# Kernel optimization log

Hardware: AMD Instinct MI355X
Metric: run time of the kernel (lower is better)

## Reference

```python
import jax, jax.numpy as jnp
import numpy as np

EPS = 1e-6

def setup_inputs() -> dict:
    key = jax.random.key(0)
    S, U, D = 512, 32, 512
    dvecs = jax.random.normal(key, (S, U, D), dtype=jnp.float32)
    w = jnp.array([10.0], dtype=jnp.float32)
    b = jnp.array([-5.0], dtype=jnp.float32)
    return {"dvecs": dvecs, "w": w, "b": b}


def _ge2e_loss(dvecs, w, b):
    S, U, D = dvecs.shape
    # Full centroids [S, D]
    centroids = dvecs.mean(axis=1)
    # Leave-one-out centroids [S, U, D] (equivalent to the roll/unfold/mean trick)
    loo = (dvecs.sum(axis=1, keepdims=True) - dvecs) / (U - 1)
    # Norms, clamped like F.cosine_similarity eps
    dn = jnp.linalg.norm(dvecs, axis=-1)        # [S, U]
    cn = jnp.linalg.norm(centroids, axis=-1)    # [S]
    ln = jnp.linalg.norm(loo, axis=-1)          # [S, U]
    # Cosine sim of every utterance vs every speaker centroid: [S, U, S]
    sim_all = jnp.einsum('sud,jd->suj', dvecs, centroids) / jnp.maximum(dn[..., None] * cn[None, None, :], EPS)
    # Self-speaker column uses the leave-one-out centroid (index_copy in torch code)
    sim_self = jnp.einsum('sud,sud->su', dvecs, loo) / jnp.maximum(dn * ln, EPS)
    spk = jnp.arange(S)
    self_mask = spk[:, None, None] == spk[None, None, :]          # [S, 1, S] -> broadcasts to [S, U, S]
    sim = jnp.where(self_mask, sim_self[..., None], sim_all)
    logits = sim * w[0] + b[0]
    losses = -jax.nn.log_softmax(logits, axis=2)                  # [S, U, S]
    # Select losses[s, u, s] and sum (index_select of diagonal entries)
    return jnp.sum(jnp.where(self_mask, losses, 0.0))


def reference(dvecs, w, b):
    return _ge2e_loss(dvecs, w, b)
```

## Files before the change

kernel.cpp:

```cpp
#include <hip/hip_runtime.h>
#include <math.h>

#define NS 512
#define NU 32
#define ND 512
#define GEPS 1e-6f

typedef float f4 __attribute__((ext_vector_type(4)));
typedef _Float16 half8 __attribute__((ext_vector_type(8)));


__global__ __launch_bounds__(256) void prep_full(const float* __restrict__ dvecs,
                                                 _Float16* __restrict__ bpk,
                                                 float* __restrict__ cn2,
                                                 float* __restrict__ dn2,
                                                 _Float16* __restrict__ apk) {
    const int s = blockIdx.x, t = threadIdx.x;
    const int l = t & 63, w = t >> 6, l15 = l & 15, lg = l >> 4;
    const int rt = w >> 1, tkh = (w & 1) * 8;
    const float* base = dvecs + (size_t)s * NU * ND;
    __shared__ float dn2p[4][16];
    __shared__ float red[4];

    const int u = rt * 16 + l15;
    const float* rowp = base + (size_t)u * ND;
    float q = 0.f;
    #pragma unroll
    for (int i = 0; i < 8; ++i) {
        const int tk = tkh + i;
        const int k0 = tk * 32 + lg * 8;
        f4 a0 = *(const f4*)(rowp + k0);
        f4 a1 = *(const f4*)(rowp + k0 + 4);
        q += a0[0]*a0[0] + a0[1]*a0[1] + a0[2]*a0[2] + a0[3]*a0[3]
           + a1[0]*a1[0] + a1[1]*a1[1] + a1[2]*a1[2] + a1[3]*a1[3];
        half8 h, lo;
        #pragma unroll
        for (int c = 0; c < 4; ++c) {
            _Float16 h0 = (_Float16)a0[c];
            h[c]     = h0; lo[c]     = (_Float16)(a0[c] - (float)h0);
            _Float16 h1 = (_Float16)a1[c];
            h[4 + c] = h1; lo[4 + c] = (_Float16)(a1[c] - (float)h1);
        }
        _Float16* cb = apk + ((size_t)(s * 2 + rt) * 16 + tk) * 1024 + l * 8;
        *(half8*)cb         = h;
        *(half8*)(cb + 512) = lo;
    }
    q += __shfl_xor(q, 16);
    q += __shfl_xor(q, 32);
    if (lg == 0) dn2p[w][l15] = q;

    const int d0 = t * 2;
    float sx = 0.f, sy = 0.f;
    #pragma unroll 4
    for (int u2 = 0; u2 < NU; ++u2) {
        float2 v = *(const float2*)(base + u2 * ND + d0);
        sx += v.x; sy += v.y;
    }
    sx *= (1.0f / NU); sy *= (1.0f / NU);
    float c2 = sx * sx + sy * sy;
    #pragma unroll
    for (int m = 1; m < 64; m <<= 1) c2 += __shfl_xor(c2, m);
    if ((t & 63) == 0) red[t >> 6] = c2;
    __syncthreads();
    if (t < 32)
        dn2[s * NU + t] = dn2p[(t >> 4) * 2][t & 15] + dn2p[(t >> 4) * 2 + 1][t & 15];
    if (t == 0) cn2[s] = red[0] + red[1] + red[2] + red[3];

    _Float16 hx = (_Float16)sx, hy = (_Float16)sy;
    _Float16 lx = (_Float16)(sx - (float)hx), ly = (_Float16)(sy - (float)hy);
    const int ct_g = s >> 4, cl15 = s & 15;
    const int tt = d0 >> 5, blg = (d0 >> 3) & 3, j = d0 & 7;
    size_t hbase = ((size_t)(ct_g * 16 + tt)) * 1024 + (blg * 16 + cl15) * 8 + j;
    unsigned hi2 = (unsigned)__builtin_bit_cast(unsigned short, hx)
                 | ((unsigned)__builtin_bit_cast(unsigned short, hy) << 16);
    unsigned lo2 = (unsigned)__builtin_bit_cast(unsigned short, lx)
                 | ((unsigned)__builtin_bit_cast(unsigned short, ly) << 16);
    *(unsigned*)(bpk + hbase)       = hi2;
    *(unsigned*)(bpk + hbase + 512) = lo2;
}

__global__ __launch_bounds__(512, 3) void ge2e_full(const _Float16* __restrict__ apk,
                                                    const _Float16* __restrict__ bpk,
                                                    const float* __restrict__ cn2,
                                                    const float* __restrict__ dn2,
                                                    const float* __restrict__ wp,
                                                    const float* __restrict__ bp,
                                                    float* __restrict__ out) {
    const int s0 = blockIdx.x * 2, tid = threadIdx.x;
    const int l = tid & 63;
    const int wv = __builtin_amdgcn_readfirstlane(tid >> 6);
    const int l15 = l & 15, lg = l >> 4;

    f4 acc[2][2][4];
    #pragma unroll
    for (int sp = 0; sp < 2; ++sp)
        #pragma unroll
        for (int rt = 0; rt < 2; ++rt)
            #pragma unroll
            for (int ct = 0; ct < 4; ++ct) acc[sp][rt][ct] = (f4){0.f, 0.f, 0.f, 0.f};

    const _Float16* Au = apk + (size_t)s0 * 32 * 1024;
    const _Float16* Bu = bpk + (size_t)(wv * 4) * 16 * 1024;
    const int voff = l * 8;

    #pragma unroll 2
    for (int t = 0; t < 16; ++t) {
        half8 bh[4], bl[4];
        #pragma unroll
        for (int ct = 0; ct < 4; ++ct) {
            const _Float16* p = Bu + (ct * 16 + t) * 1024 + voff;
            bh[ct] = *(const half8*)p;
            bl[ct] = *(const half8*)(p + 512);
        }
        #pragma unroll
        for (int sp = 0; sp < 2; ++sp) {
            half8 ah[2], al[2];
            #pragma unroll
            for (int rt = 0; rt < 2; ++rt) {
                const _Float16* p = Au + sp * 32 * 1024 + (rt * 16 + t) * 1024 + voff;
                ah[rt] = *(const half8*)p;
                al[rt] = *(const half8*)(p + 512);
            }
            __builtin_amdgcn_s_setprio(1);
            #pragma unroll
            for (int ct = 0; ct < 4; ++ct)
                #pragma unroll
                for (int rt = 0; rt < 2; ++rt) {
                    acc[sp][rt][ct] = __builtin_amdgcn_mfma_f32_16x16x32_f16(ah[rt], bh[ct], acc[sp][rt][ct], 0, 0, 0);
                    acc[sp][rt][ct] = __builtin_amdgcn_mfma_f32_16x16x32_f16(ah[rt], bl[ct], acc[sp][rt][ct], 0, 0, 0);
                    acc[sp][rt][ct] = __builtin_amdgcn_mfma_f32_16x16x32_f16(al[rt], bh[ct], acc[sp][rt][ct], 0, 0, 0);
                    acc[sp][rt][ct] = __builtin_amdgcn_mfma_f32_16x16x32_f16(al[rt], bl[ct], acc[sp][rt][ct], 0, 0, 0);
                }
            __builtin_amdgcn_s_setprio(0);
        }
    }

    __shared__ float sDn2[2][32], sSelf[2][32], sMax[2][8][32], sSum[2][8][32], sRow[2][32];
    if (tid < 64) sDn2[tid >> 5][tid & 31] = dn2[(s0 + (tid >> 5)) * NU + (tid & 31)];
    __syncthreads();

    const float w = wp[0], bb = bp[0];

    #pragma unroll
    for (int sp = 0; sp < 2; ++sp) {
        const int s = s0 + sp;
        const float cn2s = cn2[s];
        float dv[2][4];
        #pragma unroll
        for (int rt = 0; rt < 2; ++rt)
            #pragma unroll
            for (int r = 0; r < 4; ++r) dv[rt][r] = sDn2[sp][rt * 16 + lg * 4 + r];

        const bool owner = (wv == (s >> 6)) && (l15 == (s & 15));
        const int  ctd   = (s >> 4) & 3;

        float dotc[2][4];
        #pragma unroll
        for (int ct = 0; ct < 4; ++ct)
            if (ct == ctd)
                #pragma unroll
                for (int rt = 0; rt < 2; ++rt)
                    #pragma unroll
                    for (int r = 0; r < 4; ++r) dotc[rt][r] = acc[sp][rt][ct][r];

        #pragma unroll
        for (int ct = 0; ct < 4; ++ct) {
            const float cv = cn2[wv * 64 + ct * 16 + l15];
            #pragma unroll
            for (int rt = 0; rt < 2; ++rt)
                #pragma unroll
                for (int r = 0; r < 4; ++r)
                    acc[sp][rt][ct][r] = w * (acc[sp][rt][ct][r] / fmaxf(sqrtf(dv[rt][r] * cv), GEPS)) + bb;
        }
        if (owner) {
            #pragma unroll
            for (int rt = 0; rt < 2; ++rt)
                #pragma unroll
                for (int r = 0; r < 4; ++r) {
                    const float d2  = dv[rt][r];
                    const float num = (float)NU * dotc[rt][r] - d2;
                    const float X   = (float)(NU * NU) * cn2s - 2.0f * NU * dotc[rt][r] + d2;
                    const float den = fmaxf(sqrtf(d2) * sqrtf(X), GEPS * (NU - 1));
                    const float ls  = w * (num / den) + bb;
                    #pragma unroll
                    for (int ct = 0; ct < 4; ++ct)
                        if (ct == ctd) acc[sp][rt][ct][r] = ls;
                    sSelf[sp][rt * 16 + lg * 4 + r] = ls;
                }
        }

        #pragma unroll
        for (int rt = 0; rt < 2; ++rt)
            #pragma unroll
            for (int r = 0; r < 4; ++r) {
                float mx = -INFINITY;
                #pragma unroll
                for (int ct = 0; ct < 4; ++ct) mx = fmaxf(mx, acc[sp][rt][ct][r]);
                mx = fmaxf(mx, __shfl_xor(mx, 1)); mx = fmaxf(mx, __shfl_xor(mx, 2));
                mx = fmaxf(mx, __shfl_xor(mx, 4)); mx = fmaxf(mx, __shfl_xor(mx, 8));
                float se = 0.f;
                #pragma unroll
                for (int ct = 0; ct < 4; ++ct) se += expf(acc[sp][rt][ct][r] - mx);
                se += __shfl_xor(se, 1); se += __shfl_xor(se, 2);
                se += __shfl_xor(se, 4); se += __shfl_xor(se, 8);
                if (l15 == 0) {
                    sMax[sp][wv][rt * 16 + lg * 4 + r] = mx;
                    sSum[sp][wv][rt * 16 + lg * 4 + r] = se;
                }
            }
    }
    __syncthreads();

    if (tid < 64) {
        const int sp = tid >> 5, u2 = tid & 31;
        float M = -INFINITY;
        #pragma unroll
        for (int v = 0; v < 8; ++v) M = fmaxf(M, sMax[sp][v][u2]);
        float S = 0.f;
        #pragma unroll
        for (int v = 0; v < 8; ++v) S += sSum[sp][v][u2] * expf(sMax[sp][v][u2] - M);
        sRow[sp][u2] = logf(S) + M - sSelf[sp][u2];
    }
    __syncthreads();
    if (tid == 0) {
        float tot = 0.f;
        #pragma unroll
        for (int sp = 0; sp < 2; ++sp)
            #pragma unroll
            for (int u2 = 0; u2 < 32; ++u2) tot += sRow[sp][u2];
        atomicAdd(out, tot);
    }
}

extern "C" void kernel_launch(void* const* d_in, const int* in_sizes, int n_in,
                              void* d_out, int out_size, void* d_ws, size_t ws_size,
                              hipStream_t stream) {
    const float* dvecs = (const float*)d_in[0];
    const float* w     = (const float*)d_in[1];
    const float* b     = (const float*)d_in[2];
    float* out = (float*)d_out;

    const size_t bpk_b = (size_t)32 * 16 * 1024 * sizeof(_Float16);
    const size_t cn2_b = (size_t)NS * sizeof(float);
    const size_t dn2_b = (size_t)NS * NU * sizeof(float);

    char* p = (char*)d_ws;
    _Float16* bpk = (_Float16*)p;                 p += bpk_b;
    float*    cn2 = (float*)p;                    p += cn2_b;
    float*    dn2 = (float*)p;                    p += dn2_b;
    _Float16* apk = (_Float16*)p;

    hipMemsetAsync(d_out, 0, sizeof(float), stream);
    prep_full<<<NS, 256, 0, stream>>>(dvecs, bpk, cn2, dn2, apk);
    ge2e_full<<<NS / 2, 512, 0, stream>>>(apk, bpk, cn2, dn2, w, b, out);
}
```

Measured before the change: 130.6 us.

## Split prep kernel, one speaker per GEMM block, double-buffer B fragments

The fused prep kernel is split in two. One kernel packs the fp16 hi/lo A tiles and row norms over 2x more blocks, and a separate kernel computes centroids and their packed form. The main kernel now handles one speaker per block instead of two, doubling the grid to 512 blocks, and the occupancy hint rises to 4. The K loop is fully unrolled with B fragments prefetched one step ahead. This adds parallelism and latency hiding, at the cost of an extra launch, a second read of dvecs, and each block re-reading the B data for only one speaker.

```diff
diff --git a/kernel.cpp b/kernel.cpp
--- a/kernel.cpp
+++ b/kernel.cpp
@@ -10,24 +10,19 @@
 typedef _Float16 half8 __attribute__((ext_vector_type(8)));
 
 
-__global__ __launch_bounds__(256) void prep_full(const float* __restrict__ dvecs,
-                                                 _Float16* __restrict__ bpk,
-                                                 float* __restrict__ cn2,
-                                                 float* __restrict__ dn2,
-                                                 _Float16* __restrict__ apk) {
-    const int s = blockIdx.x, t = threadIdx.x;
-    const int l = t & 63, w = t >> 6, l15 = l & 15, lg = l >> 4;
-    const int rt = w >> 1, tkh = (w & 1) * 8;
-    const float* base = dvecs + (size_t)s * NU * ND;
+__global__ __launch_bounds__(256) void prep_apk(const float* __restrict__ dvecs,
+                                                float* __restrict__ dn2,
+                                                _Float16* __restrict__ apk) {
+    const int b = blockIdx.x, s = b >> 1, rt = b & 1;
+    const int t = threadIdx.x, l = t & 63, w = t >> 6, l15 = l & 15, lg = l >> 4;
+    const int u = rt * 16 + l15;
+    const float* rowp = dvecs + ((size_t)s * NU + u) * ND;
     __shared__ float dn2p[4][16];
-    __shared__ float red[4];
-
-    const int u = rt * 16 + l15;
-    const float* rowp = base + (size_t)u * ND;
+
     float q = 0.f;
     #pragma unroll
-    for (int i = 0; i < 8; ++i) {
-        const int tk = tkh + i;
+    for (int i = 0; i < 4; ++i) {
+        const int tk = w * 4 + i;
         const int k0 = tk * 32 + lg * 8;
         f4 a0 = *(const f4*)(rowp + k0);
         f4 a1 = *(const f4*)(rowp + k0 + 4);
@@ -48,22 +43,30 @@
     q += __shfl_xor(q, 16);
     q += __shfl_xor(q, 32);
     if (lg == 0) dn2p[w][l15] = q;
-
+    __syncthreads();
+    if (t < 16)
+        dn2[s * NU + rt * 16 + t] = dn2p[0][t] + dn2p[1][t] + dn2p[2][t] + dn2p[3][t];
+}
+
+__global__ __launch_bounds__(256) void prep_cent(const float* __restrict__ dvecs,
+                                                 _Float16* __restrict__ bpk,
+                                                 float* __restrict__ cn2) {
+    const int s = blockIdx.x, t = threadIdx.x;
+    const float* base = dvecs + (size_t)s * NU * ND;
     const int d0 = t * 2;
     float sx = 0.f, sy = 0.f;
     #pragma unroll 4
-    for (int u2 = 0; u2 < NU; ++u2) {
-        float2 v = *(const float2*)(base + u2 * ND + d0);
+    for (int u = 0; u < NU; ++u) {
+        float2 v = *(const float2*)(base + u * ND + d0);
         sx += v.x; sy += v.y;
     }
     sx *= (1.0f / NU); sy *= (1.0f / NU);
     float c2 = sx * sx + sy * sy;
     #pragma unroll
     for (int m = 1; m < 64; m <<= 1) c2 += __shfl_xor(c2, m);
+    __shared__ float red[4];
     if ((t & 63) == 0) red[t >> 6] = c2;
     __syncthreads();
-    if (t < 32)
-        dn2[s * NU + t] = dn2p[(t >> 4) * 2][t & 15] + dn2p[(t >> 4) * 2 + 1][t & 15];
     if (t == 0) cn2[s] = red[0] + red[1] + red[2] + red[3];
 
     _Float16 hx = (_Float16)sx, hy = (_Float16)sy;
@@ -79,45 +82,50 @@
     *(unsigned*)(bpk + hbase + 512) = lo2;
 }
 
-__global__ __launch_bounds__(512, 3) void ge2e_full(const _Float16* __restrict__ apk,
+__global__ __launch_bounds__(512, 4) void ge2e_full(const _Float16* __restrict__ apk,
                                                     const _Float16* __restrict__ bpk,
                                                     const float* __restrict__ cn2,
                                                     const float* __restrict__ dn2,
                                                     const float* __restrict__ wp,
                                                     const float* __restrict__ bp,
                                                     float* __restrict__ out) {
-    const int s0 = blockIdx.x * 2, tid = threadIdx.x;
+    const int s = blockIdx.x, tid = threadIdx.x;
     const int l = tid & 63;
     const int wv = __builtin_amdgcn_readfirstlane(tid >> 6);
     const int l15 = l & 15, lg = l >> 4;
 
-    f4 acc[2][2][4];
-    #pragma unroll
-    for (int sp = 0; sp < 2; ++sp)
-        #pragma unroll
-        for (int rt = 0; rt < 2; ++rt)
-            #pragma unroll
-            for (int ct = 0; ct < 4; ++ct) acc[sp][rt][ct] = (f4){0.f, 0.f, 0.f, 0.f};
-
-    const _Float16* Au = apk + (size_t)s0 * 32 * 1024;
+    f4 acc[2][4];
+    #pragma unroll
+    for (int rt = 0; rt < 2; ++rt)
+        #pragma unroll
+        for (int ct = 0; ct < 4; ++ct) acc[rt][ct] = (f4){0.f, 0.f, 0.f, 0.f};
+
+    const _Float16* Au = apk + (size_t)s * 32 * 1024;
     const _Float16* Bu = bpk + (size_t)(wv * 4) * 16 * 1024;
     const int voff = l * 8;
 
-    #pragma unroll 2
-    for (int t = 0; t < 16; ++t) {
-        half8 bh[4], bl[4];
+    half8 bh0[4], bl0[4], bh1[4], bl1[4];
+    #pragma unroll
+    for (int ct = 0; ct < 4; ++ct) {
+        const _Float16* p = Bu + (ct * 16 + 0) * 1024 + voff;
+        bh0[ct] = *(const half8*)p;
+        bl0[ct] = *(const half8*)(p + 512);
+    }
+
+    #pragma unroll
+    for (int tt = 0; tt < 8; ++tt) {
+        const int t0 = tt * 2, t1 = t0 + 1;
         #pragma unroll
         for (int ct = 0; ct < 4; ++ct) {
-            const _Float16* p = Bu + (ct * 16 + t) * 1024 + voff;
-            bh[ct] = *(const half8*)p;
-            bl[ct] = *(const half8*)(p + 512);
-        }
-        #pragma unroll
-        for (int sp = 0; sp < 2; ++sp) {
+            const _Float16* p = Bu + (ct * 16 + t1) * 1024 + voff;
+            bh1[ct] = *(const half8*)p;
+            bl1[ct] = *(const half8*)(p + 512);
+        }
+        {
             half8 ah[2], al[2];
             #pragma unroll
             for (int rt = 0; rt < 2; ++rt) {
-                const _Float16* p = Au + sp * 32 * 1024 + (rt * 16 + t) * 1024 + voff;
+                const _Float16* p = Au + (rt * 16 + t0) * 1024 + voff;
                 ah[rt] = *(const half8*)p;
                 al[rt] = *(const half8*)(p + 512);
             }
@@ -126,108 +134,128 @@
             for (int ct = 0; ct < 4; ++ct)
                 #pragma unroll
                 for (int rt = 0; rt < 2; ++rt) {
-                    acc[sp][rt][ct] = __builtin_amdgcn_mfma_f32_16x16x32_f16(ah[rt], bh[ct], acc[sp][rt][ct], 0, 0, 0);
-                    acc[sp][rt][ct] = __builtin_amdgcn_mfma_f32_16x16x32_f16(ah[rt], bl[ct], acc[sp][rt][ct], 0, 0, 0);
-                    acc[sp][rt][ct] = __builtin_amdgcn_mfma_f32_16x16x32_f16(al[rt], bh[ct], acc[sp][rt][ct], 0, 0, 0);
-                    acc[sp][rt][ct] = __builtin_amdgcn_mfma_f32_16x16x32_f16(al[rt], bl[ct], acc[sp][rt][ct], 0, 0, 0);
+                    acc[rt][ct] = __builtin_amdgcn_mfma_f32_16x16x32_f16(ah[rt], bh0[ct], acc[rt][ct], 0, 0, 0);
+                    acc[rt][ct] = __builtin_amdgcn_mfma_f32_16x16x32_f16(ah[rt], bl0[ct], acc[rt][ct], 0, 0, 0);
+                    acc[rt][ct] = __builtin_amdgcn_mfma_f32_16x16x32_f16(al[rt], bh0[ct], acc[rt][ct], 0, 0, 0);
+                    acc[rt][ct] = __builtin_amdgcn_mfma_f32_16x16x32_f16(al[rt], bl0[ct], acc[rt][ct], 0, 0, 0);
                 }
             __builtin_amdgcn_s_setprio(0);
         }
-    }
-
-    __shared__ float sDn2[2][32], sSelf[2][32], sMax[2][8][32], sSum[2][8][32], sRow[2][32];
-    if (tid < 64) sDn2[tid >> 5][tid & 31] = dn2[(s0 + (tid >> 5)) * NU + (tid & 31)];
+        if (tt < 7) {
+            #pragma unroll
+            for (int ct = 0; ct < 4; ++ct) {
+                const _Float16* p = Bu + (ct * 16 + t0 + 2) * 1024 + voff;
+                bh0[ct] = *(const half8*)p;
+                bl0[ct] = *(const half8*)(p + 512);
+            }
+        }
+        {
+            half8 ah[2], al[2];
+            #pragma unroll
+            for (int rt = 0; rt < 2; ++rt) {
+                const _Float16* p = Au + (rt * 16 + t1) * 1024 + voff;
+                ah[rt] = *(const half8*)p;
+                al[rt] = *(const half8*)(p + 512);
+            }
+            __builtin_amdgcn_s_setprio(1);
+            #pragma unroll
+            for (int ct = 0; ct < 4; ++ct)
+                #pragma unroll
+                for (int rt = 0; rt < 2; ++rt) {
+                    acc[rt][ct] = __builtin_amdgcn_mfma_f32_16x16x32_f16(ah[rt], bh1[ct], acc[rt][ct], 0, 0, 0);
+                    acc[rt][ct] = __builtin_amdgcn_mfma_f32_16x16x32_f16(ah[rt], bl1[ct], acc[rt][ct], 0, 0, 0);
+                    acc[rt][ct] = __builtin_amdgcn_mfma_f32_16x16x32_f16(al[rt], bh1[ct], acc[rt][ct], 0, 0, 0);
+                    acc[rt][ct] = __builtin_amdgcn_mfma_f32_16x16x32_f16(al[rt], bl1[ct], acc[rt][ct], 0, 0, 0);
+                }
+            __builtin_amdgcn_s_setprio(0);
+        }
+    }
+
+    __shared__ float sDn2[32], sSelf[32], sMax[8][32], sSum[8][32], sRow[32];
+    if (tid < 32) sDn2[tid] = dn2[s * NU + tid];
     __syncthreads();
 
     const float w = wp[0], bb = bp[0];
-
-    #pragma unroll
-    for (int sp = 0; sp < 2; ++sp) {
-        const int s = s0 + sp;
-        const float cn2s = cn2[s];
-        float dv[2][4];
+    const float cn2s = cn2[s];
+    float dv[2][4];
+    #pragma unroll
+    for (int rt = 0; rt < 2; ++rt)
+        #pragma unroll
+        for (int r = 0; r < 4; ++r) dv[rt][r] = sDn2[rt * 16 + lg * 4 + r];
+
+    const bool owner = (wv == (s >> 6)) && (l15 == (s & 15));
+    const int  ctd   = (s >> 4) & 3;
+
+    float dotc[2][4];
+    #pragma unroll
+    for (int ct = 0; ct < 4; ++ct)
+        if (ct == ctd)
+            #pragma unroll
+            for (int rt = 0; rt < 2; ++rt)
+                #pragma unroll
+                for (int r = 0; r < 4; ++r) dotc[rt][r] = acc[rt][ct][r];
+
+    #pragma unroll
+    for (int ct = 0; ct < 4; ++ct) {
+        const float cv = cn2[wv * 64 + ct * 16 + l15];
         #pragma unroll
         for (int rt = 0; rt < 2; ++rt)
             #pragma unroll
-            for (int r = 0; r < 4; ++r) dv[rt][r] = sDn2[sp][rt * 16 + lg * 4 + r];
-
-        const bool owner = (wv == (s >> 6)) && (l15 == (s & 15));
-        const int  ctd   = (s >> 4) & 3;
-
-        float dotc[2][4];
-        #pragma unroll
-        for (int ct = 0; ct < 4; ++ct)
-            if (ct == ctd)
-                #pragma unroll
-                for (int rt = 0; rt < 2; ++rt)
-                    #pragma unroll
-                    for (int r = 0; r < 4; ++r) dotc[rt][r] = acc[sp][rt][ct][r];
-
-        #pragma unroll
-        for (int ct = 0; ct < 4; ++ct) {
-            const float cv = cn2[wv * 64 + ct * 16 + l15];
-            #pragma unroll
-            for (int rt = 0; rt < 2; ++rt)
-                #pragma unroll
-                for (int r = 0; r < 4; ++r)
-                    acc[sp][rt][ct][r] = w * (acc[sp][rt][ct][r] / fmaxf(sqrtf(dv[rt][r] * cv), GEPS)) + bb;
-        }
-        if (owner) {
-            #pragma unroll
-            for (int rt = 0; rt < 2; ++rt)
-                #pragma unroll
-                for (int r = 0; r < 4; ++r) {
-                    const float d2  = dv[rt][r];
-                    const float num = (float)NU * dotc[rt][r] - d2;
-                    const float X   = (float)(NU * NU) * cn2s - 2.0f * NU * dotc[rt][r] + d2;
-                    const float den = fmaxf(sqrtf(d2) * sqrtf(X), GEPS * (NU - 1));
-                    const float ls  = w * (num / den) + bb;
-                    #pragma unroll
-                    for (int ct = 0; ct < 4; ++ct)
-                        if (ct == ctd) acc[sp][rt][ct][r] = ls;
-                    sSelf[sp][rt * 16 + lg * 4 + r] = ls;
-                }
-        }
-
+            for (int r = 0; r < 4; ++r)
+                acc[rt][ct][r] = w * (acc[rt][ct][r] / fmaxf(sqrtf(dv[rt][r] * cv), GEPS)) + bb;
+    }
+    if (owner) {
         #pragma unroll
         for (int rt = 0; rt < 2; ++rt)
             #pragma unroll
             for (int r = 0; r < 4; ++r) {
-                float mx = -INFINITY;
-                #pragma unroll
-                for (int ct = 0; ct < 4; ++ct) mx = fmaxf(mx, acc[sp][rt][ct][r]);
-                mx = fmaxf(mx, __shfl_xor(mx, 1)); mx = fmaxf(mx, __shfl_xor(mx, 2));
-                mx = fmaxf(mx, __shfl_xor(mx, 4)); mx = fmaxf(mx, __shfl_xor(mx, 8));
-                float se = 0.f;
-                #pragma unroll
-                for (int ct = 0; ct < 4; ++ct) se += expf(acc[sp][rt][ct][r] - mx);
-                se += __shfl_xor(se, 1); se += __shfl_xor(se, 2);
-                se += __shfl_xor(se, 4); se += __shfl_xor(se, 8);
-                if (l15 == 0) {
-                    sMax[sp][wv][rt * 16 + lg * 4 + r] = mx;
-                    sSum[sp][wv][rt * 16 + lg * 4 + r] = se;
-                }
-            }
-    }
-    __syncthreads();
-
-    if (tid < 64) {
-        const int sp = tid >> 5, u2 = tid & 31;
+                const float d2  = dv[rt][r];
+                const float num = (float)NU * dotc[rt][r] - d2;
+                const float X   = (float)(NU * NU) * cn2s - 2.0f * NU * dotc[rt][r] + d2;
+                const float den = fmaxf(sqrtf(d2) * sqrtf(X), GEPS * (NU - 1));
+                const float ls  = w * (num / den) + bb;
+                #pragma unroll
+                for (int ct = 0; ct < 4; ++ct)
+                    if (ct == ctd) acc[rt][ct][r] = ls;
+                sSelf[rt * 16 + lg * 4 + r] = ls;
+            }
+    }
+
+    #pragma unroll
+    for (int rt = 0; rt < 2; ++rt)
+        #pragma unroll
+        for (int r = 0; r < 4; ++r) {
+            float mx = -INFINITY;
+            #pragma unroll
+            for (int ct = 0; ct < 4; ++ct) mx = fmaxf(mx, acc[rt][ct][r]);
+            mx = fmaxf(mx, __shfl_xor(mx, 1)); mx = fmaxf(mx, __shfl_xor(mx, 2));
+            mx = fmaxf(mx, __shfl_xor(mx, 4)); mx = fmaxf(mx, __shfl_xor(mx, 8));
+            float se = 0.f;
+            #pragma unroll
+            for (int ct = 0; ct < 4; ++ct) se += expf(acc[rt][ct][r] - mx);
+            se += __shfl_xor(se, 1); se += __shfl_xor(se, 2);
+            se += __shfl_xor(se, 4); se += __shfl_xor(se, 8);
+            if (l15 == 0) {
+                sMax[wv][rt * 16 + lg * 4 + r] = mx;
+                sSum[wv][rt * 16 + lg * 4 + r] = se;
+            }
+        }
+    __syncthreads();
+
+    if (tid < 32) {
         float M = -INFINITY;
         #pragma unroll
-        for (int v = 0; v < 8; ++v) M = fmaxf(M, sMax[sp][v][u2]);
+        for (int v = 0; v < 8; ++v) M = fmaxf(M, sMax[v][tid]);
         float S = 0.f;
         #pragma unroll
-        for (int v = 0; v < 8; ++v) S += sSum[sp][v][u2] * expf(sMax[sp][v][u2] - M);
-        sRow[sp][u2] = logf(S) + M - sSelf[sp][u2];
+        for (int v = 0; v < 8; ++v) S += sSum[v][tid] * expf(sMax[v][tid] - M);
+        sRow[tid] = logf(S) + M - sSelf[tid];
     }
     __syncthreads();
     if (tid == 0) {
         float tot = 0.f;
         #pragma unroll
-        for (int sp = 0; sp < 2; ++sp)
-            #pragma unroll
-            for (int u2 = 0; u2 < 32; ++u2) tot += sRow[sp][u2];
+        for (int u2 = 0; u2 < 32; ++u2) tot += sRow[u2];
         atomicAdd(out, tot);
     }
 }
@@ -251,6 +279,7 @@
     _Float16* apk = (_Float16*)p;
 
     hipMemsetAsync(d_out, 0, sizeof(float), stream);
-    prep_full<<<NS, 256, 0, stream>>>(dvecs, bpk, cn2, dn2, apk);
-    ge2e_full<<<NS / 2, 512, 0, stream>>>(apk, bpk, cn2, dn2, w, b, out);
-}
+    prep_apk<<<NS * 2, 256, 0, stream>>>(dvecs, dn2, apk);
+    prep_cent<<<NS, 256, 0, stream>>>(dvecs, bpk, cn2);
+    ge2e_full<<<NS, 512, 0, stream>>>(apk, bpk, cn2, dn2, w, b, out);
+}
```

Measured after the change: 147.4 us. 12.8% more time.
